# Kernel optimization log

Measured on AMD Instinct MI355X. Metric: run time of the kernel, lower is better.

## Reference

```python
import jax, jax.numpy as jnp
import numpy as np

N_NODES = 8192
D_FEAT = 128
R_BITS = 8      # rows per band
B_BANDS = 64    # number of LSH bands
D_THRESH = 0.25 # cosine-distance threshold from LSH(z, d=0.25, ...)


def setup_inputs() -> dict:
    key = jax.random.key(0)
    k1, k2, k3 = jax.random.split(key, 3)
    z = jax.random.normal(k1, (N_NODES, D_FEAT), dtype=jnp.float32)
    # random hyperplanes for signed-projection LSH: r*b = 512 planes
    H = jax.random.normal(k2, (D_FEAT, R_BITS * B_BANDS), dtype=jnp.float32)
    edge_index = jax.random.randint(k3, (2, N_NODES * 16), 0, N_NODES, dtype=jnp.int64)
    return {"z": z, "H": H, "edge_index": edge_index}


def reference(z, H, edge_index):
    # edge_index is unused by forward_all (kept for signature fidelity).
    N = z.shape[0]
    # --- hyperplane LSH signatures ---
    bits = (z @ H) > 0                              # [N, r*b] bool
    bits = bits.reshape(N, B_BANDS, R_BITS)         # [N, b, r]
    powers = (2 ** jnp.arange(R_BITS)).astype(jnp.int32)
    codes = jnp.sum(bits.astype(jnp.int32) * powers, axis=-1)  # [N, b] band hash codes

    # --- candidate pairs: collide in at least one band (OR over bands) ---
    def band_or(mask, c):  # c: [N] codes for one band
        return mask | (c[:, None] == c[None, :]), None
    collide, _ = jax.lax.scan(band_or, jnp.zeros((N, N), dtype=bool), codes.T)

    # --- exact cosine similarity on candidates ---
    zn = z / jnp.linalg.norm(z, axis=1, keepdims=True)
    S = zn @ zn.T                                   # [N, N] cosine similarity
    dist = 1.0 - S                                  # cosine distance

    eye = jnp.eye(N, dtype=bool)
    # pairs kept by LSH: colliding, within distance threshold, off-diagonal
    keep = collide & (dist < D_THRESH) & (~eye)
    # adjacency[v1, v2] = 1 - dist = cos_sim (sigmoid=True path); identity on diagonal
    A = jnp.where(keep, S, 0.0) + eye.astype(S.dtype)
    return A
```

## Files before the change

### kernel.cpp

```cpp
#include <hip/hip_runtime.h>
#include <hip/hip_bf16.h>

#define N_NODES 8192
#define D_FEAT 128

#define ZN_BYTES (2u * 1024u * 1024u)
#define LIST_CAP 1024

typedef __bf16 bf16x8 __attribute__((ext_vector_type(8)));
typedef float f32x4 __attribute__((ext_vector_type(4)));

__device__ __forceinline__ void stage_barrier() {
  asm volatile("s_waitcnt vmcnt(16) lgkmcnt(0)\n\ts_barrier" ::: "memory");
}
__device__ __forceinline__ void vm0_barrier() {
  asm volatile("s_waitcnt vmcnt(0) lgkmcnt(0)\n\ts_barrier" ::: "memory");
}

__device__ __forceinline__ void async_copy16(void* lds, const void* g) {
  __builtin_amdgcn_global_load_lds(
      (const __attribute__((address_space(1))) void*)g,
      (__attribute__((address_space(3))) void*)lds, 16, 0, 0);
}

__device__ __attribute__((noinline)) bool lsh_collide(
    const float* __restrict__ z, const float* __restrict__ H, int i, int j) {
  for (int b = 0; b < 64; ++b) {
    unsigned ci = 0, cj = 0;
    for (int bit = 0; bit < 8; ++bit) {
      int col = b * 8 + bit;
      float di = 0.f, dj = 0.f;
      for (int k = 0; k < D_FEAT; ++k) {
        float h = H[(size_t)k * 512 + col];
        di += z[(size_t)i * D_FEAT + k] * h;
        dj += z[(size_t)j * D_FEAT + k] * h;
      }
      if (di > 0.f) ci |= (1u << bit);
      if (dj > 0.f) cj |= (1u << bit);
    }
    if (ci == cj) return true;
  }
  return false;
}

__device__ __forceinline__ unsigned pack_bf16x2(float x, float y) {
  __hip_bfloat16 bx = __float2bfloat16(x), by = __float2bfloat16(y);
  return (unsigned)(*(unsigned short*)&bx) |
         ((unsigned)(*(unsigned short*)&by) << 16);
}

__global__ __launch_bounds__(256) void norm_kernel(const float* __restrict__ z,
                                                   uint4* __restrict__ zn,
                                                   int* __restrict__ cnt) {
  if (blockIdx.x == 0 && threadIdx.x == 0) *cnt = 0;
  int gt = (int)blockIdx.x * 256 + (int)threadIdx.x;
  int row = gt >> 3, oct = gt & 7;
  const float4* src = (const float4*)(z + (size_t)row * D_FEAT + oct * 16);
  float4 v[4];
#pragma unroll
  for (int c = 0; c < 4; ++c) v[c] = src[c];
  float ss = 0.f;
#pragma unroll
  for (int c = 0; c < 4; ++c)
    ss += v[c].x * v[c].x + v[c].y * v[c].y + v[c].z * v[c].z + v[c].w * v[c].w;
  ss += __shfl_xor(ss, 1);
  ss += __shfl_xor(ss, 2);
  ss += __shfl_xor(ss, 4);
  float inv = rsqrtf(ss);
  int blk = row >> 7, r = row & 127;
  uint4* dst = zn + (size_t)blk * 2048 + r * 16;
#pragma unroll
  for (int c2 = 0; c2 < 2; ++c2) {
    float4 a = v[2 * c2], b = v[2 * c2 + 1];
    uint4 o;
    o.x = pack_bf16x2(a.x * inv, a.y * inv);
    o.y = pack_bf16x2(a.z * inv, a.w * inv);
    o.z = pack_bf16x2(b.x * inv, b.y * inv);
    o.w = pack_bf16x2(b.z * inv, b.w * inv);
    dst[(oct * 2 + c2) ^ (r & 15)] = o;
  }
}

__global__ __launch_bounds__(256, 2) void sim_kernel(const uint4* __restrict__ zn,
                                                     float* __restrict__ out,
                                                     int* __restrict__ cnt,
                                                     int4* __restrict__ list) {
  __shared__ __align__(16) unsigned char smem[65536];

  int tid = threadIdx.x;
  int b = (int)blockIdx.x;
  int bm0 = b & 7;
  int bn = b >> 3;

  int wv = tid >> 6, lane = tid & 63;
  int wm = (wv >> 1) * 64, wn = (wv & 1) * 64;
  int m16 = lane & 15, g = lane >> 4;

  {
    const uint4* gB = zn + (size_t)bn * 2048;
    const uint4* gA = zn + (size_t)(bm0 * 8) * 2048;
#pragma unroll
    for (int i = 0; i < 8; ++i) {
      int c = i * 256 + tid;
      async_copy16(smem + 32768 + c * 16, gB + c);
      async_copy16(smem + c * 16, gA + c);
    }
  }
  vm0_barrier();

  bf16x8 fbr[16];
  {
    unsigned short (*Bs)[128] = (unsigned short (*)[128])(smem + 32768);
#pragma unroll
    for (int kc = 0; kc < 4; ++kc) {
      int cs = ((kc * 4 + g) ^ m16) * 8;
#pragma unroll
      for (int tt = 0; tt < 4; ++tt)
        fbr[kc * 4 + tt] = *(const bf16x8*)&Bs[wn + tt * 16 + m16][cs];
    }
  }

  for (int t = 0; t < 8; ++t) {
    int bm = bm0 * 8 + t;
    unsigned char* cur = smem + (t & 1) * 32768;
    unsigned char* nxt = smem + ((t + 1) & 1) * 32768;

    stage_barrier();

    if (t < 7) {
      const uint4* gA = zn + (size_t)(bm + 1) * 2048;
#pragma unroll
      for (int i = 0; i < 8; ++i) {
        int c = i * 256 + tid;
        async_copy16(nxt + c * 16, gA + c);
      }
    }

    {
      f32x4* outq = (f32x4*)out + ((size_t)b << 15) + (size_t)t * 4096;
#pragma unroll
      for (int it = 0; it < 16; ++it) {
        int loc = it * 256 + tid;
        int row = (b << 4) + (t << 1) + (loc >> 11);
        int col0 = (loc & 2047) << 2;
        f32x4 v;
        v[0] = (col0 == row) ? 1.0f : 0.0f;
        v[1] = (col0 + 1 == row) ? 1.0f : 0.0f;
        v[2] = (col0 + 2 == row) ? 1.0f : 0.0f;
        v[3] = (col0 + 3 == row) ? 1.0f : 0.0f;
        outq[loc] = v;
      }
    }

    unsigned short (*As)[128] = (unsigned short (*)[128])cur;
    f32x4 acc[4][4] = {};
#pragma unroll
    for (int kc = 0; kc < 4; ++kc) {
      bf16x8 fa[4];
      int cs = ((kc * 4 + g) ^ m16) * 8;
#pragma unroll
      for (int tt = 0; tt < 4; ++tt)
        fa[tt] = *(const bf16x8*)&As[wm + tt * 16 + m16][cs];
#pragma unroll
      for (int tm = 0; tm < 4; ++tm)
#pragma unroll
        for (int tn = 0; tn < 4; ++tn)
          acc[tm][tn] = __builtin_amdgcn_mfma_f32_16x16x32_bf16(fa[tm], fbr[kc * 4 + tn], acc[tm][tn], 0, 0, 0);
    }

#pragma unroll
    for (int tm = 0; tm < 4; ++tm)
#pragma unroll
      for (int tn = 0; tn < 4; ++tn) {
        f32x4 c = acc[tm][tn];
        float m4 = fmaxf(fmaxf(c[0], c[1]), fmaxf(c[2], c[3]));
        if (m4 > 0.75f) {
          int j = bn * 128 + wn + tn * 16 + m16;
#pragma unroll
          for (int r = 0; r < 4; ++r) {
            int i = bm * 128 + wm + tm * 16 + g * 4 + r;
            if (i != j && c[r] > 0.75f) {
              int idx = atomicAdd(cnt, 1);
              if (idx < LIST_CAP)
                list[idx] = make_int4(i, j, __float_as_int(c[r]), 0);
            }
          }
        }
      }
  }
}

__global__ __launch_bounds__(256) void fixup_kernel(const float* __restrict__ z,
                                                    const float* __restrict__ H,
                                                    const int* __restrict__ cnt,
                                                    const int4* __restrict__ list,
                                                    float* __restrict__ out) {
  int n = *cnt;
  if (n > LIST_CAP) n = LIST_CAP;
  for (int e = (int)threadIdx.x; e < n; e += 256) {
    int i = list[e].x, j = list[e].y;
    float s = __int_as_float(list[e].z);
    if (lsh_collide(z, H, i, j)) out[(size_t)i * N_NODES + j] = s;
  }
}

extern "C" void kernel_launch(void* const* d_in, const int* in_sizes, int n_in,
                              void* d_out, int out_size, void* d_ws, size_t ws_size,
                              hipStream_t stream) {
  const float* z = (const float*)d_in[0];
  const float* H = (const float*)d_in[1];
  float* out = (float*)d_out;
  unsigned char* ws = (unsigned char*)d_ws;
  uint4* zn = (uint4*)ws;
  int* cnt = (int*)(ws + ZN_BYTES);
  int4* list = (int4*)(ws + ZN_BYTES + 16);
  (void)ws_size;

  norm_kernel<<<256, 256, 0, stream>>>(z, zn, cnt);
  sim_kernel<<<512, 256, 0, stream>>>(zn, out, cnt, list);
  fixup_kernel<<<1, 256, 0, stream>>>(z, H, cnt, list, out);
}
```

Baseline: 268.9 us.

## Exploit similarity symmetry: compute only upper-triangular tiles, split blocks into compute and fill roles

Builds a triangular schedule over 128x128 tiles so that only tiles with bm <= bn are computed. Each off-diagonal hit is emitted twice, once mirrored, which roughly halves the MFMA work. Blocks from NCOMPUTE upward only write identity/zero rows, while compute blocks write 4 row-strips each across 5 A-tiles. The cost is uneven load between the two block roles, a sqrt-based tile index decode, and more atomics per hit.

```diff
diff --git a/kernel.cpp b/kernel.cpp
--- a/kernel.cpp
+++ b/kernel.cpp
@@ -6,12 +6,13 @@
 
 #define ZN_BYTES (2u * 1024u * 1024u)
 #define LIST_CAP 1024
+#define NCOMPUTE 442
 
 typedef __bf16 bf16x8 __attribute__((ext_vector_type(8)));
 typedef float f32x4 __attribute__((ext_vector_type(4)));
 
-__device__ __forceinline__ void stage_barrier() {
-  asm volatile("s_waitcnt vmcnt(16) lgkmcnt(0)\n\ts_barrier" ::: "memory");
+__device__ __forceinline__ void stage_barrier32() {
+  asm volatile("s_waitcnt vmcnt(32) lgkmcnt(0)\n\ts_barrier" ::: "memory");
 }
 __device__ __forceinline__ void vm0_barrier() {
   asm volatile("s_waitcnt vmcnt(0) lgkmcnt(0)\n\ts_barrier" ::: "memory");
@@ -89,8 +90,33 @@
 
   int tid = threadIdx.x;
   int b = (int)blockIdx.x;
-  int bm0 = b & 7;
-  int bn = b >> 3;
+
+  if (b >= NCOMPUTE) {
+    f32x4* outq = (f32x4*)out + ((size_t)b << 15);
+#pragma unroll 8
+    for (int it = 0; it < 128; ++it) {
+      int loc = it * 256 + tid;
+      int row = (b << 4) + (loc >> 11);
+      int col0 = (loc & 2047) << 2;
+      f32x4 v;
+      v[0] = (col0 == row) ? 1.0f : 0.0f;
+      v[1] = (col0 + 1 == row) ? 1.0f : 0.0f;
+      v[2] = (col0 + 2 == row) ? 1.0f : 0.0f;
+      v[3] = (col0 + 3 == row) ? 1.0f : 0.0f;
+      outq[loc] = v;
+    }
+    return;
+  }
+
+  int a = (int)((sqrtf(40.0f * (float)b + 25.0f) - 5.0f) * 0.1f);
+  while (5 * (a + 1) * (a + 2) / 2 <= b) ++a;
+  while (a > 0 && 5 * a * (a + 1) / 2 > b) --a;
+  int rem = b - 5 * a * (a + 1) / 2;
+  int ap1 = a + 1;
+  int r = rem / ap1;
+  int c = rem - r * ap1;
+  int bn = 5 * a + r;
+  int bm0 = 5 * c;
 
   int wv = tid >> 6, lane = tid & 63;
   int wm = (wv >> 1) * 64, wn = (wv & 1) * 64;
@@ -98,12 +124,12 @@
 
   {
     const uint4* gB = zn + (size_t)bn * 2048;
-    const uint4* gA = zn + (size_t)(bm0 * 8) * 2048;
+    const uint4* gA = zn + (size_t)bm0 * 2048;
 #pragma unroll
     for (int i = 0; i < 8; ++i) {
-      int c = i * 256 + tid;
-      async_copy16(smem + 32768 + c * 16, gB + c);
-      async_copy16(smem + c * 16, gA + c);
+      int cc = i * 256 + tid;
+      async_copy16(smem + 32768 + cc * 16, gB + cc);
+      async_copy16(smem + cc * 16, gA + cc);
     }
   }
   vm0_barrier();
@@ -120,28 +146,29 @@
     }
   }
 
-  for (int t = 0; t < 8; ++t) {
-    int bm = bm0 * 8 + t;
+  for (int t = 0; t < 5; ++t) {
+    int bm = bm0 + t;
+    bool live = (bm <= bn);
     unsigned char* cur = smem + (t & 1) * 32768;
     unsigned char* nxt = smem + ((t + 1) & 1) * 32768;
 
-    stage_barrier();
-
-    if (t < 7) {
+    stage_barrier32();
+
+    if (t < 4 && bm + 1 <= bn) {
       const uint4* gA = zn + (size_t)(bm + 1) * 2048;
 #pragma unroll
       for (int i = 0; i < 8; ++i) {
-        int c = i * 256 + tid;
-        async_copy16(nxt + c * 16, gA + c);
-      }
-    }
-
-    {
-      f32x4* outq = (f32x4*)out + ((size_t)b << 15) + (size_t)t * 4096;
-#pragma unroll
-      for (int it = 0; it < 16; ++it) {
+        int cc = i * 256 + tid;
+        async_copy16(nxt + cc * 16, gA + cc);
+      }
+    }
+
+    if (t < 4) {
+      f32x4* outq = (f32x4*)out + ((size_t)b << 15) + ((size_t)t << 13);
+#pragma unroll
+      for (int it = 0; it < 32; ++it) {
         int loc = it * 256 + tid;
-        int row = (b << 4) + (t << 1) + (loc >> 11);
+        int row = (b << 4) + (t << 2) + (loc >> 11);
         int col0 = (loc & 2047) << 2;
         f32x4 v;
         v[0] = (col0 == row) ? 1.0f : 0.0f;
@@ -152,41 +179,48 @@
       }
     }
 
-    unsigned short (*As)[128] = (unsigned short (*)[128])cur;
-    f32x4 acc[4][4] = {};
-#pragma unroll
-    for (int kc = 0; kc < 4; ++kc) {
-      bf16x8 fa[4];
-      int cs = ((kc * 4 + g) ^ m16) * 8;
-#pragma unroll
-      for (int tt = 0; tt < 4; ++tt)
-        fa[tt] = *(const bf16x8*)&As[wm + tt * 16 + m16][cs];
+    if (live) {
+      unsigned short (*As)[128] = (unsigned short (*)[128])cur;
+      f32x4 acc[4][4] = {};
+#pragma unroll
+      for (int kc = 0; kc < 4; ++kc) {
+        bf16x8 fa[4];
+        int cs = ((kc * 4 + g) ^ m16) * 8;
+#pragma unroll
+        for (int tt = 0; tt < 4; ++tt)
+          fa[tt] = *(const bf16x8*)&As[wm + tt * 16 + m16][cs];
+#pragma unroll
+        for (int tm = 0; tm < 4; ++tm)
+#pragma unroll
+          for (int tn = 0; tn < 4; ++tn)
+            acc[tm][tn] = __builtin_amdgcn_mfma_f32_16x16x32_bf16(fa[tm], fbr[kc * 4 + tn], acc[tm][tn], 0, 0, 0);
+      }
+
 #pragma unroll
       for (int tm = 0; tm < 4; ++tm)
 #pragma unroll
-        for (int tn = 0; tn < 4; ++tn)
-          acc[tm][tn] = __builtin_amdgcn_mfma_f32_16x16x32_bf16(fa[tm], fbr[kc * 4 + tn], acc[tm][tn], 0, 0, 0);
-    }
-
-#pragma unroll
-    for (int tm = 0; tm < 4; ++tm)
-#pragma unroll
-      for (int tn = 0; tn < 4; ++tn) {
-        f32x4 c = acc[tm][tn];
-        float m4 = fmaxf(fmaxf(c[0], c[1]), fmaxf(c[2], c[3]));
-        if (m4 > 0.75f) {
-          int j = bn * 128 + wn + tn * 16 + m16;
-#pragma unroll
-          for (int r = 0; r < 4; ++r) {
-            int i = bm * 128 + wm + tm * 16 + g * 4 + r;
-            if (i != j && c[r] > 0.75f) {
-              int idx = atomicAdd(cnt, 1);
-              if (idx < LIST_CAP)
-                list[idx] = make_int4(i, j, __float_as_int(c[r]), 0);
+        for (int tn = 0; tn < 4; ++tn) {
+          f32x4 cc = acc[tm][tn];
+          float m4 = fmaxf(fmaxf(cc[0], cc[1]), fmaxf(cc[2], cc[3]));
+          if (m4 > 0.75f) {
+            int j = bn * 128 + wn + tn * 16 + m16;
+#pragma unroll
+            for (int rr = 0; rr < 4; ++rr) {
+              int i = bm * 128 + wm + tm * 16 + g * 4 + rr;
+              if (i != j && cc[rr] > 0.75f) {
+                int idx = atomicAdd(cnt, 1);
+                if (idx < LIST_CAP)
+                  list[idx] = make_int4(i, j, __float_as_int(cc[rr]), 0);
+                if (bm < bn) {
+                  int idx2 = atomicAdd(cnt, 1);
+                  if (idx2 < LIST_CAP)
+                    list[idx2] = make_int4(j, i, __float_as_int(cc[rr]), 0);
+                }
+              }
             }
           }
         }
-      }
+    }
   }
 }
 
```

Measured after the change: 269.1 us. No clear change (+0.1%).
